# Kernel tuning notes

Hardware: AMD Instinct MI355X
Metric: run time of the kernel (lower is better)

Reference implementation:

```python
import jax, jax.numpy as jnp
import numpy as np

B, F, E, K, O = 4096, 64, 16, 8, 32
NFEAT, HID = 100000, 1024
EPS = 1e-5
N_ITER = 50  # entmax bisection iterations (entmax package default)


def entmax15(x):
    # alpha=1.5 entmax via bisection, faithful to EntmaxBisectFunction.forward
    d = x.shape[-1]
    xs = x * 0.5  # X * (alpha - 1)
    mx = jnp.max(xs, axis=-1, keepdims=True)
    tau_lo = mx - 1.0                      # gp(1, 1.5) = 1
    tau_hi = mx - (1.0 / d) ** 0.5         # gp(1/d, 1.5)
    f_lo = jnp.sum(jnp.square(jnp.maximum(xs - tau_lo, 0.0)), -1, keepdims=True) - 1.0
    dm = tau_hi - tau_lo

    def body(i, carry):
        tau_lo, dm, _ = carry
        dm = dm * 0.5
        tau_m = tau_lo + dm
        f_m = jnp.sum(jnp.square(jnp.maximum(xs - tau_m, 0.0)), -1, keepdims=True) - 1.0
        tau_lo = jnp.where(f_m * f_lo >= 0, tau_m, tau_lo)
        return (tau_lo, dm, tau_m)

    _, _, tau_m = jax.lax.fori_loop(0, N_ITER, body, (tau_lo, dm, tau_lo))
    p = jnp.square(jnp.maximum(xs - tau_m, 0.0))
    return p / jnp.sum(p, -1, keepdims=True)


def bn_channels(x, g, b):
    # BatchNorm1d on (B, C, L): normalize over batch and L per channel C (train mode)
    m = jnp.mean(x, (0, 2), keepdims=True)
    v = jnp.var(x, (0, 2), keepdims=True)
    return (x - m) / jnp.sqrt(v + EPS) * g[None, :, None] + b[None, :, None]


def bn_feat(x, g, b):
    # BatchNorm1d on (B, C) (train mode, biased variance)
    m = jnp.mean(x, 0)
    v = jnp.var(x, 0)
    return (x - m) / jnp.sqrt(v + EPS) * g + b


def setup_inputs() -> dict:
    key = jax.random.key(0)
    ks = jax.random.split(key, 12)
    gain = 1.414
    aQ = gain * np.sqrt(6.0 / (O + E))
    aB = gain * np.sqrt(6.0 / (E + E))
    aV = gain * np.sqrt(6.0 / (O + F))
    D0 = K * O * E
    return {
        'x_id': jax.random.randint(ks[0], (B, F), 0, NFEAT),
        'x_value': jax.random.uniform(ks[1], (B, F), dtype=jnp.float32),
        'emb': jax.random.normal(ks[2], (NFEAT, E), dtype=jnp.float32) * 0.1,
        'emb_g': jnp.ones((F,), jnp.float32), 'emb_b': jnp.zeros((F,), jnp.float32),
        'Q': jax.random.uniform(ks[3], (K, O, E), jnp.float32, -aQ, aQ),
        'bil': jax.random.uniform(ks[4], (K, E, E), jnp.float32, -aB, aB),
        'vals': jax.random.uniform(ks[5], (K, O, F), jnp.float32, -aV, aV),
        'arm_g': jnp.ones((K * O,), jnp.float32), 'arm_b': jnp.zeros((K * O,), jnp.float32),
        'w1': jax.random.normal(ks[6], (HID, D0), jnp.float32) / np.sqrt(D0),
        'b1': jnp.zeros((HID,), jnp.float32),
        'g1': jnp.ones((HID,), jnp.float32), 'bt1': jnp.zeros((HID,), jnp.float32),
        'w2': jax.random.normal(ks[7], (HID, HID), jnp.float32) / np.sqrt(HID),
        'b2': jnp.zeros((HID,), jnp.float32),
        'g2': jnp.ones((HID,), jnp.float32), 'bt2': jnp.zeros((HID,), jnp.float32),
        'wout': jax.random.normal(ks[8], (1, HID), jnp.float32) / np.sqrt(HID),
        'bout': jnp.zeros((1,), jnp.float32),
    }


def reference(x_id, x_value, emb, emb_g, emb_b, Q, bil, vals, arm_g, arm_b,
              w1, b1, g1, bt1, w2, b2, g2, bt2, wout, bout):
    v = jnp.clip(x_value, 0.001, 1.0)
    xe = emb[x_id] * v[..., None]                       # B,F,E
    x_exp = bn_channels(jnp.exp(xe), emb_g, emb_b)       # B,F,E
    # bilinear attention scores + global context bias
    kq = jnp.einsum('kxy,koy->kox', bil, Q)              # K,O,E (fuse param contraction)
    sc = jnp.einsum('bfx,kox->bkof', xe, kq)             # B,K,O,F
    gc = jnp.einsum('bx,kox->bko', xe.sum(1), kq)        # B,K,O
    sg = entmax15(sc + gc[..., None])                    # B,K,O,F sparse gates
    aw = sg * vals[None]                                 # B,K,O,F
    arm = jnp.einsum('bfe,bkof->bkoe', x_exp, aw)        # B,K,O,E
    arm = arm.reshape(arm.shape[0], K * O, E)
    arm = bn_channels(arm, arm_g, arm_b).reshape(arm.shape[0], -1)
    h = jax.nn.relu(bn_feat(arm @ w1.T + b1, g1, bt1))
    h = jax.nn.relu(bn_feat(h @ w2.T + b2, g2, bt2))
    y = h @ wout.T + bout
    return y[:, 0]
```

## Files before the change

### kernel.cpp

```cpp
#include <hip/hip_runtime.h>

#define EPS 1e-5f

typedef __bf16 bf16;
typedef bf16 bf16x8 __attribute__((ext_vector_type(8)));
typedef float f32x4 __attribute__((ext_vector_type(4)));

__device__ __forceinline__ void lds_cp16(void* lds, const void* g) {
  __builtin_amdgcn_global_load_lds(
      (const __attribute__((address_space(1))) void*)g,
      (__attribute__((address_space(3))) void*)lds, 16, 0, 0);
}

__device__ __forceinline__ f32x4 mfma_bf16(bf16x8 a, bf16x8 b, f32x4 c) {
  return __builtin_amdgcn_mfma_f32_16x16x32_bf16(a, b, c, 0, 0, 0);
}

__global__ void k_embed(const int* __restrict__ x_id, const float* __restrict__ x_val,
                        const float* __restrict__ emb, float* __restrict__ xe,
                        float* __restrict__ es_p, float* __restrict__ eq_p) {
  int t = threadIdx.x, bid = blockIdx.x;
  float s = 0.f, q = 0.f;
#pragma unroll
  for (int it = 0; it < 4; ++it) {
    int g = it * 65536 + bid * 256 + t;
    int id = x_id[g];
    float v = fminf(fmaxf(x_val[g], 0.001f), 1.0f);
    const float4* er = (const float4*)(emb + (size_t)id * 16);
    float4* xo = (float4*)(xe + (size_t)g * 16);
#pragma unroll
    for (int j = 0; j < 4; ++j) {
      float4 e = er[j];
      e.x *= v; e.y *= v; e.z *= v; e.w *= v;
      xo[j] = e;
      float a0 = __expf(e.x), a1 = __expf(e.y), a2 = __expf(e.z), a3 = __expf(e.w);
      s += (a0 + a1) + (a2 + a3);
      q += (a0 * a0 + a1 * a1) + (a2 * a2 + a3 * a3);
    }
  }
  __shared__ float rs[256], rq[256];
  rs[t] = s; rq[t] = q;
  __syncthreads();
  if (t < 64) {
    float S = rs[t] + rs[t + 64] + rs[t + 128] + rs[t + 192];
    float Q = rq[t] + rq[t + 64] + rq[t + 128] + rq[t + 192];
    es_p[bid * 64 + t] = S;
    eq_p[bid * 64 + t] = Q;
  }
}

__global__ void k_prep(const float* __restrict__ Qw, const float* __restrict__ bil,
                       bf16* __restrict__ kqh, bf16* __restrict__ kql,
                       const float* __restrict__ es_p, const float* __restrict__ eq_p,
                       const float* __restrict__ g_, const float* __restrict__ b_,
                       float* __restrict__ oa, float* __restrict__ ob) {
  int t = threadIdx.x;
  int k = t >> 5;
  float qv[16];
#pragma unroll
  for (int y = 0; y < 16; ++y) qv[y] = Qw[t * 16 + y];
  const float* bl = bil + k * 256;
#pragma unroll
  for (int x = 0; x < 16; ++x) {
    float s = 0.f;
#pragma unroll
    for (int y = 0; y < 16; ++y) s += bl[x * 16 + y] * qv[y];
    s *= 0.5f;
    bf16 h = (bf16)s;
    kqh[t * 16 + x] = h;
    kql[t * 16 + x] = (bf16)(s - (float)h);
  }
  if (t < 64) {
    float S = 0.f, Q = 0.f;
    for (int i = 0; i < 256; ++i) { S += es_p[i * 64 + t]; Q += eq_p[i * 64 + t]; }
    float mean = S * (1.0f / 65536.0f);
    float var = Q * (1.0f / 65536.0f) - mean * mean;
    float a = g_[t] * rsqrtf(var + EPS);
    oa[t] = a;
    ob[t] = b_[t] - mean * a;
  }
}

__global__ __launch_bounds__(256, 3) void k_attn(
    const float* __restrict__ xe_g, const bf16* __restrict__ kqh_g,
    const bf16* __restrict__ kql_g, const float* __restrict__ eba,
    const float* __restrict__ ebb, const float* __restrict__ vals,
    bf16* __restrict__ arm) {
  __shared__ __align__(16) unsigned char smem[47424];
  bf16* s_aw = (bf16*)smem;
  float* s_xe = (float*)smem;
  bf16* s_X = (bf16*)(smem + 36864);
  bf16* s_Ah = (bf16*)(smem + 39168);
  bf16* s_Al = (bf16*)(smem + 43264);
  float* s_sum = (float*)(smem + 47360);
  const int t = threadIdx.x;
  const int b = blockIdx.x;
  const int w = t >> 6, lane = t & 63;
  const int q = lane >> 4, ln = lane & 15;
  const f32x4 z4 = {0.f, 0.f, 0.f, 0.f};

  ((float4*)s_xe)[t] = ((const float4*)(xe_g + (size_t)b * 1024))[t];
  __syncthreads();

  if (t < 16) {
    float s = 0.f;
#pragma unroll
    for (int f = 0; f < 64; ++f) s += s_xe[f * 16 + t];
    s_sum[t] = s;
  }
  {
    int f = t >> 2, e0 = (t & 3) * 4;
    float a = eba[f], c = ebb[f];
#pragma unroll
    for (int j = 0; j < 4; ++j) {
      float v = __expf(s_xe[f * 16 + e0 + j]) * a + c;
      s_X[(e0 + j) * 72 + f] = (bf16)v;
    }
  }
  __syncthreads();

  {
    int f = t >> 2, x0 = (t & 3) * 4;
    union { bf16 h[4]; unsigned long long u; } ph, pl, pz;
    pz.u = 0ull;
#pragma unroll
    for (int j = 0; j < 4; ++j) {
      float v = s_xe[f * 16 + x0 + j] + s_sum[x0 + j];
      bf16 h = (bf16)v;
      ph.h[j] = h;
      pl.h[j] = (bf16)(v - (float)h);
    }
    *(unsigned long long*)(s_Ah + f * 32 + x0) = ph.u;
    *(unsigned long long*)(s_Al + f * 32 + x0) = pl.u;
    *(unsigned long long*)(s_Ah + f * 32 + 16 + x0) = pz.u;
    *(unsigned long long*)(s_Al + f * 32 + 16 + x0) = pz.u;
  }
  __syncthreads();

  bf16x8 Ah[4], Al[4];
#pragma unroll
  for (int ft = 0; ft < 4; ++ft) {
    int row = ft * 16 + ln;
    Ah[ft] = *(const bf16x8*)(s_Ah + row * 32 + q * 8);
    Al[ft] = *(const bf16x8*)(s_Al + row * 32 + q * 8);
  }

#pragma unroll
  for (int gi = 0; gi < 4; ++gi) {
    const int ko = (w * 4 + gi) * 16 + ln;
    bf16x8 Bh, Bl;
#pragma unroll
    for (int j = 0; j < 8; ++j) { Bh[j] = (bf16)0.f; Bl[j] = (bf16)0.f; }
    if (q < 2) {
      Bh = *(const bf16x8*)(kqh_g + ko * 16 + q * 8);
      Bl = *(const bf16x8*)(kql_g + ko * 16 + q * 8);
    }
    f32x4 xs[4];
#pragma unroll
    for (int ft = 0; ft < 4; ++ft) {
      f32x4 a = z4;
      a = mfma_bf16(Ah[ft], Bh, a);
      a = mfma_bf16(Al[ft], Bh, a);
      a = mfma_bf16(Ah[ft], Bl, a);
      xs[ft] = a;
    }

    f32x4 mm = __builtin_elementwise_max(__builtin_elementwise_max(xs[0], xs[1]),
                                         __builtin_elementwise_max(xs[2], xs[3]));
    float mx = fmaxf(fmaxf(mm.x, mm.y), fmaxf(mm.z, mm.w));
    mx = fmaxf(mx, __shfl_xor(mx, 16, 64));
    mx = fmaxf(mx, __shfl_xor(mx, 32, 64));

    float tau_lo = mx - 1.0f;
    float dm = 0.875f;
#pragma unroll
    for (int it = 0; it < 7; ++it) {
      dm *= 0.5f;
      float tm = tau_lo + dm;
      f32x4 t4 = {tm, tm, tm, tm};
      f32x4 c4 = z4;
#pragma unroll
      for (int ft = 0; ft < 4; ++ft) {
        f32x4 d = __builtin_elementwise_max(xs[ft] - t4, z4);
        c4 += d * d;
      }
      float s = (c4.x + c4.y) + (c4.z + c4.w);
      s += __shfl_xor(s, 16, 64);
      s += __shfl_xor(s, 32, 64);
      tau_lo = (s - 1.0f >= 0.f) ? tm : tau_lo;
    }
    float tau = tau_lo + dm;
#pragma unroll
    for (int r = 0; r < 2; ++r) {
      f32x4 t4 = {tau, tau, tau, tau};
      f32x4 S4 = z4, Q4 = z4;
      float cnt = 0.f;
#pragma unroll
      for (int ft = 0; ft < 4; ++ft) {
        f32x4 y = xs[ft] - t4;
        f32x4 m = __builtin_elementwise_max(y, z4);
        S4 += m; Q4 += m * m;
        cnt += (y.x > 0.f ? 1.f : 0.f) + (y.y > 0.f ? 1.f : 0.f) +
               (y.z > 0.f ? 1.f : 0.f) + (y.w > 0.f ? 1.f : 0.f);
      }
      float S1 = (S4.x + S4.y) + (S4.z + S4.w);
      float Q1 = (Q4.x + Q4.y) + (Q4.z + Q4.w);
      S1 += __shfl_xor(S1, 16, 64); S1 += __shfl_xor(S1, 32, 64);
      Q1 += __shfl_xor(Q1, 16, 64); Q1 += __shfl_xor(Q1, 32, 64);
      cnt += __shfl_xor(cnt, 16, 64); cnt += __shfl_xor(cnt, 32, 64);
      float disc = fmaxf(S1 * S1 - cnt * (Q1 - 1.0f), 0.f);
      tau += (S1 - sqrtf(disc)) / cnt;
    }
    f32x4 t4 = {tau, tau, tau, tau};
    f32x4 Z4 = z4;
#pragma unroll
    for (int ft = 0; ft < 4; ++ft) {
      f32x4 d = __builtin_elementwise_max(xs[ft] - t4, z4);
      f32x4 p = d * d;
      xs[ft] = p;
      Z4 += p;
    }
    float Z = (Z4.x + Z4.y) + (Z4.z + Z4.w);
    Z += __shfl_xor(Z, 16, 64);
    Z += __shfl_xor(Z, 32, 64);
    float inv = 1.0f / Z;

#pragma unroll
    for (int ft = 0; ft < 4; ++ft) {
      int f0 = ft * 16 + q * 4;
      float4 vv = *(const float4*)(vals + ko * 64 + f0);
      union { bf16 h[4]; unsigned long long u; } pk;
      pk.h[0] = (bf16)(xs[ft].x * inv * vv.x);
      pk.h[1] = (bf16)(xs[ft].y * inv * vv.y);
      pk.h[2] = (bf16)(xs[ft].z * inv * vv.z);
      pk.h[3] = (bf16)(xs[ft].w * inv * vv.w);
      *(unsigned long long*)(s_aw + ko * 72 + f0) = pk.u;
    }
  }
  __syncthreads();

  f32x4 acc[4];
#pragma unroll
  for (int mt = 0; mt < 4; ++mt) acc[mt] = z4;
#pragma unroll
  for (int ks = 0; ks < 2; ++ks) {
    bf16x8 bfrag = *(const bf16x8*)(s_X + ln * 72 + ks * 32 + q * 8);
#pragma unroll
    for (int mt = 0; mt < 4; ++mt) {
      int row = (w * 4 + mt) * 16 + ln;
      bf16x8 afrag = *(const bf16x8*)(s_aw + row * 72 + ks * 32 + q * 8);
      acc[mt] = mfma_bf16(afrag, bfrag, acc[mt]);
    }
  }
  bf16* armb = arm + (size_t)b * 4096;
#pragma unroll
  for (int mt = 0; mt < 4; ++mt) {
    int ko0 = (w * 4 + mt) * 16 + q * 4;
#pragma unroll
    for (int r = 0; r < 4; ++r)
      armb[(ko0 + r) * 16 + ln] = (bf16)acc[mt][r];
  }
}

__global__ void k_armstats(const bf16* __restrict__ arm, float* __restrict__ as_p,
                           float* __restrict__ aq_p) {
  int t = threadIdx.x;
  int b0 = blockIdx.x * 64;
  float s = 0.f, q = 0.f;
  for (int i = 0; i < 64; ++i) {
    const bf16* p = arm + (size_t)(b0 + i) * 4096 + t * 16;
    bf16x8 v0 = *(const bf16x8*)p;
    bf16x8 v1 = *(const bf16x8*)(p + 8);
#pragma unroll
    for (int j = 0; j < 8; ++j) {
      float a = (float)v0[j], c = (float)v1[j];
      s += a + c; q += a * a + c * c;
    }
  }
  as_p[blockIdx.x * 256 + t] = s;
  aq_p[blockIdx.x * 256 + t] = q;
}

__global__ void k_cvtw(const float* __restrict__ w1, const float* __restrict__ w2,
                       const float* __restrict__ as_p, const float* __restrict__ aq_p,
                       const float* __restrict__ arm_g, bf16* __restrict__ d1,
                       bf16* __restrict__ d2) {
  int t = threadIdx.x, bid = blockIdx.x;
  if (bid < 256) {
    __shared__ float scale[256];
    float s = 0.f, q = 0.f;
    for (int i = 0; i < 64; ++i) { s += as_p[i * 256 + t]; q += aq_p[i * 256 + t]; }
    float mean = s * (1.0f / 65536.0f);
    float var = q * (1.0f / 65536.0f) - mean * mean;
    scale[t] = arm_g[t] * rsqrtf(var + EPS);
    __syncthreads();
#pragma unroll
    for (int it = 0; it < 16; ++it) {
      int i = it * 65536 + bid * 256 + t;
      float4 v = ((const float4*)w1)[i];
      float av = scale[(i >> 2) & 255];
      union { bf16 h[4]; uint2 u; } p;
      p.h[0] = (bf16)(v.x * av); p.h[1] = (bf16)(v.y * av);
      p.h[2] = (bf16)(v.z * av); p.h[3] = (bf16)(v.w * av);
      *(uint2*)(d1 + (size_t)i * 4) = p.u;
    }
  } else {
#pragma unroll
    for (int it = 0; it < 16; ++it) {
      int i = it * 16384 + (bid - 256) * 256 + t;
      float4 v = ((const float4*)w2)[i];
      union { bf16 h[4]; uint2 u; } p;
      p.h[0] = (bf16)v.x; p.h[1] = (bf16)v.y; p.h[2] = (bf16)v.z; p.h[3] = (bf16)v.w;
      *(uint2*)(d2 + (size_t)i * 4) = p.u;
    }
  }
}

__global__ __launch_bounds__(256, 2) void gemm_bt(
    const bf16* __restrict__ A, const bf16* __restrict__ Bw, float* __restrict__ C,
    float* __restrict__ sp, float* __restrict__ sq, int Kd) {
  __shared__ __align__(16) bf16 sA[128 * 32];
  __shared__ __align__(16) bf16 sB[64 * 32];
  __shared__ float sredS[4][64], sredQ[4][64];
  const int t = threadIdx.x;
  const int w = t >> 6, lane = t & 63;
  const int m0 = blockIdx.x * 128, n0 = blockIdx.y * 64;

  f32x4 acc[2][4];
#pragma unroll
  for (int i = 0; i < 2; ++i)
#pragma unroll
    for (int j = 0; j < 4; ++j) acc[i][j] = (f32x4){0.f, 0.f, 0.f, 0.f};

  for (int kt = 0; kt < Kd; kt += 32) {
#pragma unroll
    for (int c = 0; c < 2; ++c) {
      int idx = c * 256 + t;
      int row = idx >> 2, ch = idx & 3;
      int sch = ch ^ ((row >> 1) & 3);
      lds_cp16(sA + idx * 8, A + (size_t)(m0 + row) * Kd + kt + sch * 8);
    }
    {
      int row = t >> 2, ch = t & 3;
      int sch = ch ^ ((row >> 1) & 3);
      lds_cp16(sB + t * 8, Bw + (size_t)(n0 + row) * Kd + kt + sch * 8);
    }
    __syncthreads();
    bf16x8 af[2], bfr[4];
#pragma unroll
    for (int mt = 0; mt < 2; ++mt) {
      int row = w * 32 + mt * 16 + (lane & 15);
      int ch = (lane >> 4) ^ ((row >> 1) & 3);
      af[mt] = *(const bf16x8*)(sA + row * 32 + ch * 8);
    }
#pragma unroll
    for (int nt = 0; nt < 4; ++nt) {
      int row = nt * 16 + (lane & 15);
      int ch = (lane >> 4) ^ ((row >> 1) & 3);
      bfr[nt] = *(const bf16x8*)(sB + row * 32 + ch * 8);
    }
#pragma unroll
    for (int mt = 0; mt < 2; ++mt)
#pragma unroll
      for (int nt = 0; nt < 4; ++nt)
        acc[mt][nt] = mfma_bf16(af[mt], bfr[nt], acc[mt][nt]);
    __syncthreads();
  }

#pragma unroll
  for (int nt = 0; nt < 4; ++nt) {
    int ncol = n0 + nt * 16 + (lane & 15);
    float s = 0.f, q = 0.f;
#pragma unroll
    for (int mt = 0; mt < 2; ++mt) {
      int mr = m0 + w * 32 + mt * 16 + (lane >> 4) * 4;
#pragma unroll
      for (int r = 0; r < 4; ++r) {
        float v = acc[mt][nt][r];
        C[(size_t)(mr + r) * 1024 + ncol] = v;
        s += v; q += v * v;
      }
    }
    s += __shfl_xor(s, 16, 64); s += __shfl_xor(s, 32, 64);
    q += __shfl_xor(q, 16, 64); q += __shfl_xor(q, 32, 64);
    if (lane < 16) { sredS[w][nt * 16 + lane] = s; sredQ[w][nt * 16 + lane] = q; }
  }
  __syncthreads();
  if (t < 64) {
    float S = sredS[0][t] + sredS[1][t] + sredS[2][t] + sredS[3][t];
    float Q = sredQ[0][t] + sredQ[1][t] + sredQ[2][t] + sredQ[3][t];
    sp[blockIdx.x * 1024 + n0 + t] = S;
    sq[blockIdx.x * 1024 + n0 + t] = Q;
  }
}

__global__ void k_colfin(const float* __restrict__ sp, const float* __restrict__ sq,
                         const float* __restrict__ g_, const float* __restrict__ bt,
                         float* __restrict__ a, float* __restrict__ c) {
  int h = blockIdx.x * 256 + threadIdx.x;
  float S = 0.f, Q = 0.f;
  for (int i = 0; i < 32; ++i) { S += sp[i * 1024 + h]; Q += sq[i * 1024 + h]; }
  float mean = S * (1.0f / 4096.0f);
  float var = Q * (1.0f / 4096.0f) - mean * mean;
  float av = g_[h] * rsqrtf(var + EPS);
  a[h] = av;
  c[h] = bt[h] - mean * av;
}

__global__ void k_h1bf(const float* __restrict__ C1, const float* __restrict__ a,
                       const float* __restrict__ c, bf16* __restrict__ H1) {
  int i4 = blockIdx.x * 256 + threadIdx.x;
  int col0 = (i4 * 4) & 1023;
  float4 v = ((const float4*)C1)[i4];
  float4 av = *(const float4*)(a + col0);
  float4 cv = *(const float4*)(c + col0);
  union { bf16 h[4]; uint2 u; } pk;
  pk.h[0] = (bf16)fmaxf(v.x * av.x + cv.x, 0.f);
  pk.h[1] = (bf16)fmaxf(v.y * av.y + cv.y, 0.f);
  pk.h[2] = (bf16)fmaxf(v.z * av.z + cv.z, 0.f);
  pk.h[3] = (bf16)fmaxf(v.w * av.w + cv.w, 0.f);
  *(uint2*)(H1 + (size_t)i4 * 4) = pk.u;
}

__global__ __launch_bounds__(256) void k_out(const float* __restrict__ C2,
                                             const float* __restrict__ a,
                                             const float* __restrict__ c,
                                             const float* __restrict__ wout,
                                             const float* __restrict__ bout,
                                             float* __restrict__ y) {
  int t = threadIdx.x;
  int w = t >> 6, lane = t & 63;
  int row = blockIdx.x * 4 + w;
  const float* cr = C2 + (size_t)row * 1024;
  float s = 0.f;
#pragma unroll
  for (int j = 0; j < 16; ++j) {
    int col = j * 64 + lane;
    float v = fmaxf(cr[col] * a[col] + c[col], 0.f);
    s += v * wout[col];
  }
#pragma unroll
  for (int off = 32; off > 0; off >>= 1) s += __shfl_xor(s, off, 64);
  if (lane == 0) y[row] = s + bout[0];
}

extern "C" void kernel_launch(void* const* d_in, const int* in_sizes, int n_in,
                              void* d_out, int out_size, void* d_ws, size_t ws_size,
                              hipStream_t stream) {
  (void)in_sizes; (void)n_in; (void)out_size; (void)ws_size;
  const int* x_id = (const int*)d_in[0];
  const float* x_value = (const float*)d_in[1];
  const float* emb = (const float*)d_in[2];
  const float* emb_g = (const float*)d_in[3];
  const float* embb = (const float*)d_in[4];
  const float* Qw = (const float*)d_in[5];
  const float* bil = (const float*)d_in[6];
  const float* vals = (const float*)d_in[7];
  const float* arm_g = (const float*)d_in[8];
  const float* w1 = (const float*)d_in[10];
  const float* g1 = (const float*)d_in[12];
  const float* bt1 = (const float*)d_in[13];
  const float* w2 = (const float*)d_in[14];
  const float* g2 = (const float*)d_in[16];
  const float* bt2 = (const float*)d_in[17];
  const float* wout = (const float*)d_in[18];
  const float* bout = (const float*)d_in[19];

  char* w = (char*)d_ws;
  float* ws_A = (float*)w;
  bf16* ws_arm = (bf16*)(w + 16777216);
  bf16* ws_w1b = (bf16*)(w + 50331648);
  bf16* ws_H1 = ws_w1b;
  bf16* ws_w2b = (bf16*)(w + 58720256);
  bf16* ws_kqh = (bf16*)(w + 60817408);
  bf16* ws_kql = (bf16*)(w + 60825600);
  float* misc = (float*)(w + 60833792);
  float* es_p = misc;
  float* eq_p = es_p + 16384;
  float* as_p = eq_p + 16384;
  float* aq_p = as_p + 16384;
  float* sp1 = aq_p + 16384;
  float* sq1 = sp1 + 32768;
  float* sp2 = sq1 + 32768;
  float* sq2 = sp2 + 32768;
  float* eb_a = sq2 + 32768;
  float* eb_b = eb_a + 64;
  float* a1c = eb_b + 64;
  float* c1c = a1c + 1024;
  float* a2c = c1c + 1024;
  float* c2c = a2c + 1024;

  k_embed<<<256, 256, 0, stream>>>(x_id, x_value, emb, ws_A, es_p, eq_p);
  k_prep<<<1, 256, 0, stream>>>(Qw, bil, ws_kqh, ws_kql, es_p, eq_p, emb_g, embb,
                                eb_a, eb_b);
  k_attn<<<4096, 256, 0, stream>>>(ws_A, ws_kqh, ws_kql, eb_a, eb_b, vals, ws_arm);
  k_armstats<<<64, 256, 0, stream>>>(ws_arm, as_p, aq_p);
  k_cvtw<<<320, 256, 0, stream>>>(w1, w2, as_p, aq_p, arm_g, ws_w1b, ws_w2b);
  gemm_bt<<<dim3(32, 16), 256, 0, stream>>>(ws_arm, ws_w1b, ws_A, sp1, sq1, 4096);
  k_colfin<<<4, 256, 0, stream>>>(sp1, sq1, g1, bt1, a1c, c1c);
  k_h1bf<<<4096, 256, 0, stream>>>(ws_A, a1c, c1c, ws_H1);
  gemm_bt<<<dim3(32, 16), 256, 0, stream>>>(ws_H1, ws_w2b, ws_A, sp2, sq2, 1024);
  k_colfin<<<4, 256, 0, stream>>>(sp2, sq2, g2, bt2, a2c, c2c);
  k_out<<<1024, 256, 0, stream>>>(ws_A, a2c, c2c, wout, bout, (float*)d_out);
}
```

Measured before the change: 339.6 us.

## Make entmax rows thread-local via LDS staging and double GEMM K-tile

The attention kernel now writes the MFMA score tiles to shared memory. Each thread then reads back one full 64-wide row and runs the entmax bisection, Newton refinement and normalisation on it without any cross-lane shuffles. This removes the many shuffle reductions per bisection step, at the cost of larger LDS use and fewer blocks per CU (launch bounds 3→2) plus higher register pressure. Separately, the GEMM K-tile grows from 32 to 64 with an 8-way XOR swizzle, halving the barrier and loop overhead per K element in exchange for more LDS.

```diff
diff --git a/kernel.cpp b/kernel.cpp
--- a/kernel.cpp
+++ b/kernel.cpp
@@ -5,6 +5,7 @@
 typedef __bf16 bf16;
 typedef bf16 bf16x8 __attribute__((ext_vector_type(8)));
 typedef float f32x4 __attribute__((ext_vector_type(4)));
+typedef float f32x2 __attribute__((ext_vector_type(2)));
 
 __device__ __forceinline__ void lds_cp16(void* lds, const void* g) {
   __builtin_amdgcn_global_load_lds(
@@ -81,23 +82,25 @@
   }
 }
 
-__global__ __launch_bounds__(256, 3) void k_attn(
+__global__ __launch_bounds__(256, 2) void k_attn(
     const float* __restrict__ xe_g, const bf16* __restrict__ kqh_g,
     const bf16* __restrict__ kql_g, const float* __restrict__ eba,
     const float* __restrict__ ebb, const float* __restrict__ vals,
     bf16* __restrict__ arm) {
-  __shared__ __align__(16) unsigned char smem[47424];
+  __shared__ __align__(16) unsigned char smem[80192];
+  float* s_sc = (float*)smem;
+  float* s_xe = (float*)smem;
   bf16* s_aw = (bf16*)smem;
-  float* s_xe = (float*)smem;
-  bf16* s_X = (bf16*)(smem + 36864);
-  bf16* s_Ah = (bf16*)(smem + 39168);
-  bf16* s_Al = (bf16*)(smem + 43264);
-  float* s_sum = (float*)(smem + 47360);
+  bf16* s_X = (bf16*)(smem + 69632);
+  bf16* s_Ah = (bf16*)(smem + 71936);
+  bf16* s_Al = (bf16*)(smem + 76032);
+  float* s_sum = (float*)(smem + 80128);
   const int t = threadIdx.x;
   const int b = blockIdx.x;
   const int w = t >> 6, lane = t & 63;
   const int q = lane >> 4, ln = lane & 15;
   const f32x4 z4 = {0.f, 0.f, 0.f, 0.f};
+  const f32x2 z2 = {0.f, 0.f};
 
   ((float4*)s_xe)[t] = ((const float4*)(xe_g + (size_t)b * 1024))[t];
   __syncthreads();
@@ -155,87 +158,90 @@
       Bh = *(const bf16x8*)(kqh_g + ko * 16 + q * 8);
       Bl = *(const bf16x8*)(kql_g + ko * 16 + q * 8);
     }
-    f32x4 xs[4];
 #pragma unroll
     for (int ft = 0; ft < 4; ++ft) {
       f32x4 a = z4;
       a = mfma_bf16(Ah[ft], Bh, a);
       a = mfma_bf16(Al[ft], Bh, a);
       a = mfma_bf16(Ah[ft], Bl, a);
-      xs[ft] = a;
-    }
-
-    f32x4 mm = __builtin_elementwise_max(__builtin_elementwise_max(xs[0], xs[1]),
-                                         __builtin_elementwise_max(xs[2], xs[3]));
-    float mx = fmaxf(fmaxf(mm.x, mm.y), fmaxf(mm.z, mm.w));
-    mx = fmaxf(mx, __shfl_xor(mx, 16, 64));
-    mx = fmaxf(mx, __shfl_xor(mx, 32, 64));
-
-    float tau_lo = mx - 1.0f;
-    float dm = 0.875f;
-#pragma unroll
-    for (int it = 0; it < 7; ++it) {
-      dm *= 0.5f;
-      float tm = tau_lo + dm;
-      f32x4 t4 = {tm, tm, tm, tm};
-      f32x4 c4 = z4;
-#pragma unroll
-      for (int ft = 0; ft < 4; ++ft) {
-        f32x4 d = __builtin_elementwise_max(xs[ft] - t4, z4);
-        c4 += d * d;
-      }
-      float s = (c4.x + c4.y) + (c4.z + c4.w);
-      s += __shfl_xor(s, 16, 64);
-      s += __shfl_xor(s, 32, 64);
-      tau_lo = (s - 1.0f >= 0.f) ? tm : tau_lo;
-    }
-    float tau = tau_lo + dm;
-#pragma unroll
-    for (int r = 0; r < 2; ++r) {
-      f32x4 t4 = {tau, tau, tau, tau};
-      f32x4 S4 = z4, Q4 = z4;
-      float cnt = 0.f;
-#pragma unroll
-      for (int ft = 0; ft < 4; ++ft) {
-        f32x4 y = xs[ft] - t4;
-        f32x4 m = __builtin_elementwise_max(y, z4);
-        S4 += m; Q4 += m * m;
-        cnt += (y.x > 0.f ? 1.f : 0.f) + (y.y > 0.f ? 1.f : 0.f) +
-               (y.z > 0.f ? 1.f : 0.f) + (y.w > 0.f ? 1.f : 0.f);
-      }
-      float S1 = (S4.x + S4.y) + (S4.z + S4.w);
-      float Q1 = (Q4.x + Q4.y) + (Q4.z + Q4.w);
-      S1 += __shfl_xor(S1, 16, 64); S1 += __shfl_xor(S1, 32, 64);
-      Q1 += __shfl_xor(Q1, 16, 64); Q1 += __shfl_xor(Q1, 32, 64);
-      cnt += __shfl_xor(cnt, 16, 64); cnt += __shfl_xor(cnt, 32, 64);
-      float disc = fmaxf(S1 * S1 - cnt * (Q1 - 1.0f), 0.f);
-      tau += (S1 - sqrtf(disc)) / cnt;
-    }
-    f32x4 t4 = {tau, tau, tau, tau};
-    f32x4 Z4 = z4;
-#pragma unroll
-    for (int ft = 0; ft < 4; ++ft) {
-      f32x4 d = __builtin_elementwise_max(xs[ft] - t4, z4);
-      f32x4 p = d * d;
-      xs[ft] = p;
-      Z4 += p;
-    }
-    float Z = (Z4.x + Z4.y) + (Z4.z + Z4.w);
-    Z += __shfl_xor(Z, 16, 64);
-    Z += __shfl_xor(Z, 32, 64);
-    float inv = 1.0f / Z;
-
-#pragma unroll
-    for (int ft = 0; ft < 4; ++ft) {
-      int f0 = ft * 16 + q * 4;
-      float4 vv = *(const float4*)(vals + ko * 64 + f0);
-      union { bf16 h[4]; unsigned long long u; } pk;
-      pk.h[0] = (bf16)(xs[ft].x * inv * vv.x);
-      pk.h[1] = (bf16)(xs[ft].y * inv * vv.y);
-      pk.h[2] = (bf16)(xs[ft].z * inv * vv.z);
-      pk.h[3] = (bf16)(xs[ft].w * inv * vv.w);
-      *(unsigned long long*)(s_aw + ko * 72 + f0) = pk.u;
-    }
+      *(f32x4*)(s_sc + ko * 68 + ft * 16 + q * 4) = a;
+    }
+  }
+  __syncthreads();
+
+  f32x2 xs2[32];
+#pragma unroll
+  for (int i = 0; i < 16; ++i) {
+    f32x4 v = *(const f32x4*)(s_sc + t * 68 + i * 4);
+    xs2[2 * i] = __builtin_shufflevector(v, v, 0, 1);
+    xs2[2 * i + 1] = __builtin_shufflevector(v, v, 2, 3);
+  }
+  __syncthreads();
+
+  f32x2 m2 = xs2[0];
+#pragma unroll
+  for (int i = 1; i < 32; ++i) m2 = __builtin_elementwise_max(m2, xs2[i]);
+  float mx = fmaxf(m2.x, m2.y);
+
+  float tau_lo = mx - 1.0f;
+  float dm = 0.875f;
+#pragma unroll
+  for (int it = 0; it < 7; ++it) {
+    dm *= 0.5f;
+    float tm = tau_lo + dm;
+    f32x2 t2 = {tm, tm};
+    f32x2 c2 = z2;
+#pragma unroll
+    for (int i = 0; i < 32; ++i) {
+      f32x2 d = __builtin_elementwise_max(xs2[i] - t2, z2);
+      c2 += d * d;
+    }
+    tau_lo = ((c2.x + c2.y) - 1.0f >= 0.f) ? tm : tau_lo;
+  }
+  float tau = tau_lo + dm;
+#pragma unroll
+  for (int r = 0; r < 2; ++r) {
+    f32x2 t2 = {tau, tau};
+    f32x2 S2 = z2, Q2 = z2;
+    float cnt = 0.f;
+#pragma unroll
+    for (int i = 0; i < 32; ++i) {
+      f32x2 y = xs2[i] - t2;
+      f32x2 m = __builtin_elementwise_max(y, z2);
+      S2 += m; Q2 += m * m;
+      cnt += (y.x > 0.f ? 1.f : 0.f) + (y.y > 0.f ? 1.f : 0.f);
+    }
+    float S1 = S2.x + S2.y, Q1 = Q2.x + Q2.y;
+    float disc = fmaxf(S1 * S1 - cnt * (Q1 - 1.0f), 0.f);
+    tau += (S1 - sqrtf(disc)) / cnt;
+  }
+  f32x2 Zv = z2;
+  {
+    f32x2 t2 = {tau, tau};
+#pragma unroll
+    for (int i = 0; i < 32; ++i) {
+      f32x2 d = __builtin_elementwise_max(xs2[i] - t2, z2);
+      f32x2 p = d * d;
+      xs2[i] = p;
+      Zv += p;
+    }
+  }
+  float inv = 1.0f / (Zv.x + Zv.y);
+
+  const float4* vg = (const float4*)(vals + t * 64);
+#pragma unroll
+  for (int f8 = 0; f8 < 64; f8 += 8) {
+    float4 v0 = vg[f8 / 4], v1 = vg[f8 / 4 + 1];
+    union { bf16 h[8]; uint4 u; } pk;
+    pk.h[0] = (bf16)(xs2[f8 / 2].x * inv * v0.x);
+    pk.h[1] = (bf16)(xs2[f8 / 2].y * inv * v0.y);
+    pk.h[2] = (bf16)(xs2[f8 / 2 + 1].x * inv * v0.z);
+    pk.h[3] = (bf16)(xs2[f8 / 2 + 1].y * inv * v0.w);
+    pk.h[4] = (bf16)(xs2[f8 / 2 + 2].x * inv * v1.x);
+    pk.h[5] = (bf16)(xs2[f8 / 2 + 2].y * inv * v1.y);
+    pk.h[6] = (bf16)(xs2[f8 / 2 + 3].x * inv * v1.z);
+    pk.h[7] = (bf16)(xs2[f8 / 2 + 3].y * inv * v1.w);
+    *(uint4*)(s_aw + t * 72 + f8) = pk.u;
   }
   __syncthreads();
 
@@ -319,8 +325,8 @@
 __global__ __launch_bounds__(256, 2) void gemm_bt(
     const bf16* __restrict__ A, const bf16* __restrict__ Bw, float* __restrict__ C,
     float* __restrict__ sp, float* __restrict__ sq, int Kd) {
-  __shared__ __align__(16) bf16 sA[128 * 32];
-  __shared__ __align__(16) bf16 sB[64 * 32];
+  __shared__ __align__(16) bf16 sA[128 * 64];
+  __shared__ __align__(16) bf16 sB[64 * 64];
   __shared__ float sredS[4][64], sredQ[4][64];
   const int t = threadIdx.x;
   const int w = t >> 6, lane = t & 63;
@@ -332,38 +338,43 @@
 #pragma unroll
     for (int j = 0; j < 4; ++j) acc[i][j] = (f32x4){0.f, 0.f, 0.f, 0.f};
 
-  for (int kt = 0; kt < Kd; kt += 32) {
+  for (int kt = 0; kt < Kd; kt += 64) {
+#pragma unroll
+    for (int c = 0; c < 4; ++c) {
+      int idx = c * 256 + t;
+      int row = idx >> 3, ch = idx & 7;
+      int sch = ch ^ (row & 7);
+      lds_cp16(sA + idx * 8, A + (size_t)(m0 + row) * Kd + kt + sch * 8);
+    }
 #pragma unroll
     for (int c = 0; c < 2; ++c) {
       int idx = c * 256 + t;
-      int row = idx >> 2, ch = idx & 3;
-      int sch = ch ^ ((row >> 1) & 3);
-      lds_cp16(sA + idx * 8, A + (size_t)(m0 + row) * Kd + kt + sch * 8);
-    }
-    {
-      int row = t >> 2, ch = t & 3;
-      int sch = ch ^ ((row >> 1) & 3);
-      lds_cp16(sB + t * 8, Bw + (size_t)(n0 + row) * Kd + kt + sch * 8);
+      int row = idx >> 3, ch = idx & 7;
+      int sch = ch ^ (row & 7);
+      lds_cp16(sB + idx * 8, Bw + (size_t)(n0 + row) * Kd + kt + sch * 8);
     }
     __syncthreads();
-    bf16x8 af[2], bfr[4];
-#pragma unroll
-    for (int mt = 0; mt < 2; ++mt) {
-      int row = w * 32 + mt * 16 + (lane & 15);
-      int ch = (lane >> 4) ^ ((row >> 1) & 3);
-      af[mt] = *(const bf16x8*)(sA + row * 32 + ch * 8);
-    }
-#pragma unroll
-    for (int nt = 0; nt < 4; ++nt) {
-      int row = nt * 16 + (lane & 15);
-      int ch = (lane >> 4) ^ ((row >> 1) & 3);
-      bfr[nt] = *(const bf16x8*)(sB + row * 32 + ch * 8);
-    }
-#pragma unroll
-    for (int mt = 0; mt < 2; ++mt)
-#pragma unroll
-      for (int nt = 0; nt < 4; ++nt)
-        acc[mt][nt] = mfma_bf16(af[mt], bfr[nt], acc[mt][nt]);
+#pragma unroll
+    for (int ks = 0; ks < 2; ++ks) {
+      bf16x8 af[2], bfr[4];
+#pragma unroll
+      for (int mt = 0; mt < 2; ++mt) {
+        int row = w * 32 + mt * 16 + (lane & 15);
+        int slot = (ks * 4 + (lane >> 4)) ^ (row & 7);
+        af[mt] = *(const bf16x8*)(sA + row * 64 + slot * 8);
+      }
+#pragma unroll
+      for (int nt = 0; nt < 4; ++nt) {
+        int row = nt * 16 + (lane & 15);
+        int slot = (ks * 4 + (lane >> 4)) ^ (row & 7);
+        bfr[nt] = *(const bf16x8*)(sB + row * 64 + slot * 8);
+      }
+#pragma unroll
+      for (int mt = 0; mt < 2; ++mt)
+#pragma unroll
+        for (int nt = 0; nt < 4; ++nt)
+          acc[mt][nt] = mfma_bf16(af[mt], bfr[nt], acc[mt][nt]);
+    }
     __syncthreads();
   }
 
```

Result: no change. 334.7 us (-1.4%).
